# Optimization experiments

Hardware: AMD Instinct MI355X
Metric: run time of the kernel (lower is better)

## Reference

```python
import jax, jax.numpy as jnp
import numpy as np

# Model dims (GatedAttentionLayer of Qwen3.5 ANE hybrid stack)
C = 2048      # hidden_size
H = 16        # num_attention_heads
HK = 4        # num_key_value_heads
D = 128       # head_dim
ROT = 32      # rotary_dim = head_dim * partial_rotary_factor (0.25)
S = 1024      # sequence length (prefill)
CTX = 1024    # kv cache context length
N_ATTN = 6    # number of full-attention layers -> kv_cache leading dim 2*N_ATTN
EPS = 1e-6
ROPE_THETA = 1e7


def _rotate_half(x):
    h = x.shape[-1] // 2
    return jnp.concatenate([-x[..., h:], x[..., :h]], axis=-1)


def _rms_norm(x, w, eps=EPS):
    # Qwen3.5 convention: stored weight is (w - 1), applied as (1 + weight)
    r = jax.lax.rsqrt(jnp.mean(x * x, axis=-1, keepdims=True) + eps)
    return x * r * (1.0 + w)


def setup_inputs() -> dict:
    key = jax.random.key(0)
    ks = jax.random.split(key, 6)
    hidden_states = jax.random.normal(ks[0], (1, C, 1, S), jnp.float32)
    q_proj_w = jax.random.normal(ks[1], (H * 2 * D, C), jnp.float32) * 0.02  # q + gate
    k_proj_w = jax.random.normal(ks[2], (HK * D, C), jnp.float32) * 0.02
    v_proj_w = jax.random.normal(ks[3], (HK * D, C), jnp.float32) * 0.02
    o_proj_w = jax.random.normal(ks[4], (C, H * D), jnp.float32) * 0.02
    q_norm_w = jnp.zeros((D,), jnp.float32)
    k_norm_w = jnp.zeros((D,), jnp.float32)
    kv_cache = jnp.zeros((2 * N_ATTN, HK, CTX, D), jnp.float32)
    position_ids = jnp.arange(S, dtype=jnp.int32)
    # causal mask: 0 on/below diagonal, -1e9 above
    causal_mask = jnp.where(
        jnp.arange(CTX)[None, :] <= jnp.arange(S)[:, None], 0.0, -1e9
    ).astype(jnp.float32)[None, None]  # [1,1,S,CTX]
    # RoPE tables over rotary_dim
    inv_freq = 1.0 / (ROPE_THETA ** (jnp.arange(0, ROT, 2, dtype=jnp.float32) / ROT))
    t = jnp.arange(CTX, dtype=jnp.float32)
    freqs = jnp.outer(t, inv_freq)          # [CTX, ROT//2]
    emb = jnp.concatenate([freqs, freqs], -1)  # [CTX, ROT]
    cos_cached = jnp.cos(emb)
    sin_cached = jnp.sin(emb)
    return dict(hidden_states=hidden_states, q_proj_w=q_proj_w, k_proj_w=k_proj_w,
                v_proj_w=v_proj_w, o_proj_w=o_proj_w, q_norm_w=q_norm_w,
                k_norm_w=k_norm_w, kv_cache=kv_cache, causal_mask=causal_mask,
                position_ids=position_ids, cos_cached=cos_cached,
                sin_cached=sin_cached, attn_layer_idx=0)


def reference(hidden_states, q_proj_w, k_proj_w, v_proj_w, o_proj_w,
              q_norm_w, k_norm_w, kv_cache, causal_mask, position_ids,
              cos_cached, sin_cached, attn_layer_idx):
    x = hidden_states[0, :, 0, :]                     # [C, S]
    q_raw = q_proj_w @ x                              # [H*2D, S]  (1x1 Conv2d == GEMM)
    qg = q_raw.reshape(H, 2 * D, S)
    q = jnp.transpose(qg[:, :D, :], (0, 2, 1))        # [H, S, D]
    gate = jnp.transpose(qg[:, D:, :], (0, 2, 1))     # [H, S, D]
    k = jnp.transpose((k_proj_w @ x).reshape(HK, D, S), (0, 2, 1))  # [HK, S, D]
    v = jnp.transpose((v_proj_w @ x).reshape(HK, D, S), (0, 2, 1))  # [HK, S, D]

    q = _rms_norm(q, q_norm_w)
    k = _rms_norm(k, k_norm_w)

    cos = cos_cached[position_ids]   # [S, ROT]
    sin = sin_cached[position_ids]

    def rope(t):
        rot, pas = t[..., :ROT], t[..., ROT:]
        rot = rot * cos + _rotate_half(rot) * sin
        return jnp.concatenate([rot, pas], axis=-1)

    q, k = rope(q), rope(k)

    # prefill cache write at pos_start = position_ids[0]
    k_idx = 2 * attn_layer_idx
    v_idx = k_idx + 1
    pos_start = position_ids[0]
    kv_cache = jax.lax.dynamic_update_slice(kv_cache, k[None], (k_idx, 0, pos_start, 0))
    kv_cache = jax.lax.dynamic_update_slice(kv_cache, v[None], (v_idx, 0, pos_start, 0))

    g = H // HK  # GQA repeat (expand+reshape == contiguous repeat)
    k_full = jnp.repeat(kv_cache[k_idx], g, axis=0)   # [H, CTX, D]
    v_full = jnp.repeat(kv_cache[v_idx], g, axis=0)   # [H, CTX, D]

    scale = D ** -0.5
    attn = jnp.einsum('hsd,htd->hst', q, k_full) * scale + causal_mask[0]
    attn = jax.nn.softmax(attn, axis=-1)
    out = jnp.einsum('hst,htd->hsd', attn, v_full)    # [H, S, D]
    out = out * jax.nn.sigmoid(gate)
    out = jnp.transpose(out, (0, 2, 1)).reshape(H * D, S)
    output = (o_proj_w @ out)[None, :, None, :]       # [1, C, 1, S]
    return output
```

## Files before the change

### kernel.cpp

```cpp
#include <hip/hip_runtime.h>
#include <cstdint>

#define S_LEN 1024
#define C_DIM 2048
#define NH    16
#define NHK   4
#define HD    128
#define ROT   32
#define SCALE 0.08838834764831845f

typedef __bf16 bf16x8 __attribute__((ext_vector_type(8)));
typedef float floatx4 __attribute__((ext_vector_type(4)));
typedef float floatx16 __attribute__((ext_vector_type(16)));
typedef unsigned short ushortx8 __attribute__((ext_vector_type(8)));

__device__ __forceinline__ unsigned short f2bf(float f) {
  union { float f; uint32_t u; } x; x.f = f;
  uint32_t r = (x.u + 0x7fffu + ((x.u >> 16) & 1u)) >> 16;
  return (unsigned short)r;
}
__device__ __forceinline__ float bf2f(unsigned short v) {
  union { uint32_t u; float f; } x; x.u = (uint32_t)v << 16; return x.f;
}

__device__ __forceinline__ void async_copy16(const unsigned short* g, unsigned short* l) {
  __builtin_amdgcn_global_load_lds(
      (const __attribute__((address_space(1))) void*)g,
      (__attribute__((address_space(3))) void*)l,
      16, 0, 0);
}

__global__ void cast_all_kernel(const float* __restrict__ qw, const float* __restrict__ kw,
                                const float* __restrict__ vw, const float* __restrict__ ow,
                                unsigned short* __restrict__ out) {
  const int NQ = 4096 * 2048 / 4, NK = 512 * 2048 / 4, NV = 512 * 2048 / 4;
  int i = blockIdx.x * blockDim.x + threadIdx.x;
  const float* src; int j;
  if (i < NQ) { src = qw; j = i; }
  else if (i < NQ + NK) { src = kw; j = i - NQ; }
  else if (i < NQ + NK + NV) { src = vw; j = i - NQ - NK; }
  else { src = ow; j = i - NQ - NK - NV; }
  float4 v = ((const float4*)src)[j];
  ushort4 o;
  o.x = f2bf(v.x); o.y = f2bf(v.y); o.z = f2bf(v.z); o.w = f2bf(v.w);
  ((ushort4*)out)[i] = o;
}

__global__ __launch_bounds__(256)
void transpose_cast_x_kernel(const float* __restrict__ x, unsigned short* __restrict__ xT) {
  __shared__ float t[32][33];
  int st = blockIdx.x, ct = blockIdx.y;
  int c = threadIdx.x & 31, rq = threadIdx.x >> 5;
#pragma unroll
  for (int i = 0; i < 4; ++i) {
    int r = rq + i * 8;
    t[r][c] = x[(size_t)(ct * 32 + r) * S_LEN + st * 32 + c];
  }
  __syncthreads();
#pragma unroll
  for (int i = 0; i < 4; ++i) {
    int r = rq + i * 8;
    xT[(size_t)(st * 32 + r) * C_DIM + ct * 32 + c] = f2bf(t[c][r]);
  }
}

__device__ __forceinline__ void norm_rope_epi(
    floatx16 (&acc)[2], float (*pp)[32],
    const float* __restrict__ w, const int* __restrict__ pos_ids,
    const float* __restrict__ cosc, const float* __restrict__ sinc,
    unsigned short* __restrict__ outp,
    int wave, int lane, int wm, int scol0) {
  int l31 = lane & 31, half = lane >> 5;
  float s = 0.f;
#pragma unroll
  for (int mi = 0; mi < 2; ++mi)
#pragma unroll
    for (int reg = 0; reg < 16; ++reg) { float v = acc[mi][reg]; s += v * v; }
  s += __shfl_xor(s, 32);
  if (half == 0) pp[wave][l31] = s;
  __syncthreads();
  float rn = rsqrtf((pp[wave][l31] + pp[wave ^ 1][l31]) * (1.0f / 128.0f) + 1e-6f);
  int scol = scol0 + l31;
  int pos = pos_ids[scol];
#pragma unroll
  for (int mi = 0; mi < 2; ++mi) {
    bool rope = (wm == 0) && (mi == 0);
#pragma unroll
    for (int g = 0; g < 4; ++g) {
      int dbase = wm + mi * 32 + half * 4 + g * 8;
      ushort4 o;
#pragma unroll
      for (int rr = 0; rr < 4; ++rr) {
        int reg = g * 4 + rr;
        int d = dbase + rr;
        float v = acc[mi][reg] * rn * (1.0f + w[d]);
        if (rope) {
          float cv = cosc[pos * ROT + d], sv = sinc[pos * ROT + d];
          int d2 = (d < 16) ? d + 16 : d - 16;
          float pv = acc[mi][reg ^ 8] * rn * (1.0f + w[d2]);
          v = v * cv + ((d < 16) ? -pv : pv) * sv;
        }
        ((unsigned short*)&o)[rr] = f2bf(v);
      }
      *(ushort4*)&outp[(size_t)scol * HD + dbase] = o;
    }
  }
}

__global__ __launch_bounds__(256, 4)
void gemm_qkv_fused(const unsigned short* __restrict__ A,
                    const unsigned short* __restrict__ BT,
                    const float* __restrict__ qw, const float* __restrict__ kw,
                    const int* __restrict__ pos_ids,
                    const float* __restrict__ cosc, const float* __restrict__ sinc,
                    unsigned short* __restrict__ qb, unsigned short* __restrict__ kbuf,
                    unsigned short* __restrict__ vTb, unsigned short* __restrict__ sgb) {
  __shared__ unsigned short Asm[2][128 * 64];
  __shared__ unsigned short Bsm[2][64 * 64];
  __shared__ float pp[4][32];
  int tid = threadIdx.x, wave = tid >> 6, lane = tid & 63;
  int l31 = lane & 31, half = lane >> 5;
  int wm = (wave & 1) * 64, wn = (wave >> 1) * 32;
  int m0 = blockIdx.x * 128, n0 = blockIdx.y * 64;
  int r8 = lane >> 3, c8 = lane & 7;
  int arow[4], brow[2], apos[4], bpos[2];
#pragma unroll
  for (int i = 0; i < 4; ++i) { arow[i] = wave * 32 + i * 8 + r8; apos[i] = c8 ^ (arow[i] & 7); }
#pragma unroll
  for (int i = 0; i < 2; ++i) { brow[i] = wave * 16 + i * 8 + r8; bpos[i] = c8 ^ (brow[i] & 7); }
  const unsigned short* Ag = A + (size_t)m0 * C_DIM;
  const unsigned short* Bg = BT + (size_t)n0 * C_DIM;
  floatx16 acc[2];
  acc[0] = (floatx16)0.f; acc[1] = (floatx16)0.f;
  ushortx8 rA[4], rB[2];

#pragma unroll
  for (int i = 0; i < 4; ++i) rA[i] = *(const ushortx8*)(Ag + (size_t)arow[i] * C_DIM + c8 * 8);
#pragma unroll
  for (int i = 0; i < 2; ++i) rB[i] = *(const ushortx8*)(Bg + (size_t)brow[i] * C_DIM + c8 * 8);
#pragma unroll
  for (int i = 0; i < 4; ++i) *(ushortx8*)&Asm[0][arow[i] * 64 + apos[i] * 8] = rA[i];
#pragma unroll
  for (int i = 0; i < 2; ++i) *(ushortx8*)&Bsm[0][brow[i] * 64 + bpos[i] * 8] = rB[i];
  __syncthreads();

  for (int t = 0; t < 32; ++t) {
    int b = t & 1;
    if (t < 31) {
      int kt = (t + 1) * 64;
#pragma unroll
      for (int i = 0; i < 4; ++i) rA[i] = *(const ushortx8*)(Ag + (size_t)arow[i] * C_DIM + kt + c8 * 8);
#pragma unroll
      for (int i = 0; i < 2; ++i) rB[i] = *(const ushortx8*)(Bg + (size_t)brow[i] * C_DIM + kt + c8 * 8);
    }
#pragma unroll
    for (int kb = 0; kb < 4; ++kb) {
      int co = (((kb << 1) | half) ^ (l31 & 7)) << 3;
      bf16x8 a0 = *(const bf16x8*)&Asm[b][(wm + l31) * 64 + co];
      bf16x8 a1 = *(const bf16x8*)&Asm[b][(wm + 32 + l31) * 64 + co];
      bf16x8 bf = *(const bf16x8*)&Bsm[b][(wn + l31) * 64 + co];
      acc[0] = __builtin_amdgcn_mfma_f32_32x32x16_bf16(a0, bf, acc[0], 0, 0, 0);
      acc[1] = __builtin_amdgcn_mfma_f32_32x32x16_bf16(a1, bf, acc[1], 0, 0, 0);
    }
    if (t < 31) {
#pragma unroll
      for (int i = 0; i < 4; ++i) *(ushortx8*)&Asm[b ^ 1][arow[i] * 64 + apos[i] * 8] = rA[i];
#pragma unroll
      for (int i = 0; i < 2; ++i) *(ushortx8*)&Bsm[b ^ 1][brow[i] * 64 + bpos[i] * 8] = rB[i];
    }
    __syncthreads();
  }

  int scol0 = n0 + wn;
  int ty = blockIdx.x;
  if (ty < 32) {
    int h = ty >> 1;
    if ((ty & 1) == 0) {
      norm_rope_epi(acc, pp, qw, pos_ids, cosc, sinc,
                    qb + (size_t)h * S_LEN * HD, wave, lane, wm, scol0);
    } else {
      int scol = scol0 + l31;
#pragma unroll
      for (int mi = 0; mi < 2; ++mi)
#pragma unroll
        for (int g = 0; g < 4; ++g) {
          int dbase = wm + mi * 32 + half * 4 + g * 8;
          ushort4 o;
#pragma unroll
          for (int rr = 0; rr < 4; ++rr)
            ((unsigned short*)&o)[rr] = f2bf(1.0f / (1.0f + __expf(-acc[mi][g * 4 + rr])));
          *(ushort4*)&sgb[((size_t)h * S_LEN + scol) * HD + dbase] = o;
        }
    }
  } else if (ty < 36) {
    int hk = ty - 32;
    norm_rope_epi(acc, pp, kw, pos_ids, cosc, sinc,
                  kbuf + (size_t)hk * S_LEN * HD, wave, lane, wm, scol0);
  } else {
    int hk = ty - 36;
#pragma unroll
    for (int mi = 0; mi < 2; ++mi)
#pragma unroll
      for (int reg = 0; reg < 16; ++reg) {
        int d = wm + mi * 32 + (reg & 3) + 8 * (reg >> 2) + 4 * half;
        vTb[(size_t)hk * HD * S_LEN + (size_t)d * S_LEN + scol0 + l31] = f2bf(acc[mi][reg]);
      }
  }
}

__global__ __launch_bounds__(256, 4)
void gemm_oproj(const unsigned short* __restrict__ A,
                const unsigned short* __restrict__ BT,
                float* __restrict__ C) {
  __shared__ unsigned short Asm[2][128 * 64];
  __shared__ unsigned short Bsm[2][64 * 64];
  int tid = threadIdx.x, wave = tid >> 6, lane = tid & 63;
  int l31 = lane & 31, half = lane >> 5;
  int wm = (wave & 1) * 64, wn = (wave >> 1) * 32;
  int m0 = blockIdx.x * 128, n0 = blockIdx.y * 64;
  int r8 = lane >> 3, c8 = lane & 7;
  int arow[4], brow[2], apos[4], bpos[2];
#pragma unroll
  for (int i = 0; i < 4; ++i) { arow[i] = wave * 32 + i * 8 + r8; apos[i] = c8 ^ (arow[i] & 7); }
#pragma unroll
  for (int i = 0; i < 2; ++i) { brow[i] = wave * 16 + i * 8 + r8; bpos[i] = c8 ^ (brow[i] & 7); }
  const unsigned short* Ag = A + (size_t)m0 * C_DIM;
  const unsigned short* Bg = BT + (size_t)n0 * C_DIM;
  floatx16 acc[2];
  acc[0] = (floatx16)0.f; acc[1] = (floatx16)0.f;
  ushortx8 rA[4], rB[2];

#pragma unroll
  for (int i = 0; i < 4; ++i) rA[i] = *(const ushortx8*)(Ag + (size_t)arow[i] * C_DIM + c8 * 8);
#pragma unroll
  for (int i = 0; i < 2; ++i) rB[i] = *(const ushortx8*)(Bg + (size_t)brow[i] * C_DIM + c8 * 8);
#pragma unroll
  for (int i = 0; i < 4; ++i) *(ushortx8*)&Asm[0][arow[i] * 64 + apos[i] * 8] = rA[i];
#pragma unroll
  for (int i = 0; i < 2; ++i) *(ushortx8*)&Bsm[0][brow[i] * 64 + bpos[i] * 8] = rB[i];
  __syncthreads();

  for (int t = 0; t < 32; ++t) {
    int b = t & 1;
    if (t < 31) {
      int kt = (t + 1) * 64;
#pragma unroll
      for (int i = 0; i < 4; ++i) rA[i] = *(const ushortx8*)(Ag + (size_t)arow[i] * C_DIM + kt + c8 * 8);
#pragma unroll
      for (int i = 0; i < 2; ++i) rB[i] = *(const ushortx8*)(Bg + (size_t)brow[i] * C_DIM + kt + c8 * 8);
    }
#pragma unroll
    for (int kb = 0; kb < 4; ++kb) {
      int co = (((kb << 1) | half) ^ (l31 & 7)) << 3;
      bf16x8 a0 = *(const bf16x8*)&Asm[b][(wm + l31) * 64 + co];
      bf16x8 a1 = *(const bf16x8*)&Asm[b][(wm + 32 + l31) * 64 + co];
      bf16x8 bf = *(const bf16x8*)&Bsm[b][(wn + l31) * 64 + co];
      acc[0] = __builtin_amdgcn_mfma_f32_32x32x16_bf16(a0, bf, acc[0], 0, 0, 0);
      acc[1] = __builtin_amdgcn_mfma_f32_32x32x16_bf16(a1, bf, acc[1], 0, 0, 0);
    }
    if (t < 31) {
#pragma unroll
      for (int i = 0; i < 4; ++i) *(ushortx8*)&Asm[b ^ 1][arow[i] * 64 + apos[i] * 8] = rA[i];
#pragma unroll
      for (int i = 0; i < 2; ++i) *(ushortx8*)&Bsm[b ^ 1][brow[i] * 64 + bpos[i] * 8] = rB[i];
    }
    __syncthreads();
  }
#pragma unroll
  for (int mi = 0; mi < 2; ++mi)
#pragma unroll
    for (int reg = 0; reg < 16; ++reg) {
      int row = m0 + wm + mi * 32 + (reg & 3) + 8 * (reg >> 2) + 4 * half;
      C[(size_t)row * S_LEN + n0 + wn + l31] = acc[mi][reg];
    }
}

__global__ __launch_bounds__(256)
void attn_kernel(const unsigned short* __restrict__ qb,
                 const unsigned short* __restrict__ kbuf,
                 const unsigned short* __restrict__ vTb,
                 const unsigned short* __restrict__ sgb,
                 unsigned short* __restrict__ outT) {
  __shared__ __align__(16) unsigned short Ks[64 * 128];
  __shared__ __align__(16) unsigned short Vs[128 * 64];
  __shared__ __align__(16) unsigned short Ps[4][16][72];
  int h = blockIdx.x, qt = blockIdx.y;
  int s0 = qt * 64;
  int hk = h >> 2;
  int tid = threadIdx.x, wave = tid >> 6, lane = tid & 63;
  int l16 = lane & 15, quad = lane >> 4;
  int lsw = l16 & 7;

  const unsigned short* qg = qb + ((size_t)(h * S_LEN + s0 + wave * 16 + l16)) * HD;
  bf16x8 qfr[4];
#pragma unroll
  for (int kb = 0; kb < 4; ++kb)
    qfr[kb] = *(const bf16x8*)(qg + kb * 32 + quad * 8);

  float m_r[4], l_r[4];
#pragma unroll
  for (int r = 0; r < 4; ++r) { m_r[r] = -1e30f; l_r[r] = 0.f; }
  floatx4 acc_o[8];
#pragma unroll
  for (int i = 0; i < 8; ++i) acc_o[i] = (floatx4)0.f;
  int srow_base = s0 + wave * 16 + quad * 4;

  const unsigned short* kg0 = kbuf + (size_t)hk * S_LEN * HD;
  const unsigned short* vg0 = vTb + (size_t)hk * HD * S_LEN;

  int kr4 = lane >> 4, kc16 = lane & 15;
  int vr8 = lane >> 3, vc8 = lane & 7;

  for (int t = 0; t <= qt; ++t) {
    int jt = t * 64;
#pragma unroll
    for (int i = 0; i < 4; ++i) {
      int rbase = wave * 16 + i * 4;
      int row = rbase + kr4;
      int cs = kc16 ^ (row & 7);
      async_copy16(kg0 + (size_t)(jt + row) * HD + cs * 8, Ks + rbase * 128);
    }
#pragma unroll
    for (int i = 0; i < 4; ++i) {
      int rbase = wave * 32 + i * 8;
      int row = rbase + vr8;
      int cs = vc8 ^ (row & 7);
      async_copy16(vg0 + (size_t)row * S_LEN + jt + cs * 8, Vs + rbase * 64);
    }
    __syncthreads();

    floatx4 acc_s[4];
#pragma unroll
    for (int ni = 0; ni < 4; ++ni) acc_s[ni] = (floatx4)0.f;
#pragma unroll
    for (int kb = 0; kb < 4; ++kb) {
#pragma unroll
      for (int ni = 0; ni < 4; ++ni) {
        int cl = (kb * 4 + quad) ^ lsw;
        bf16x8 bk = *(const bf16x8*)&Ks[(ni * 16 + l16) * 128 + cl * 8];
        acc_s[ni] = __builtin_amdgcn_mfma_f32_16x16x32_bf16(qfr[kb], bk, acc_s[ni], 0, 0, 0);
      }
    }

    bool diag = (t == qt);
    float alpha[4];
#pragma unroll
    for (int r = 0; r < 4; ++r) {
      float scv[4];
      float mx = -1e30f;
#pragma unroll
      for (int ni = 0; ni < 4; ++ni) {
        float sv = acc_s[ni][r] * SCALE;
        if (diag) {
          int jg = jt + ni * 16 + l16;
          if (jg > srow_base + r) sv = -1e30f;
        }
        scv[ni] = sv;
        mx = fmaxf(mx, sv);
      }
#pragma unroll
      for (int off = 8; off; off >>= 1) mx = fmaxf(mx, __shfl_xor(mx, off, 16));
      float mnew = fmaxf(m_r[r], mx);
      float psv = 0.f;
#pragma unroll
      for (int ni = 0; ni < 4; ++ni) {
        float pv = (scv[ni] > -1e29f) ? __expf(scv[ni] - mnew) : 0.f;
        Ps[wave][quad * 4 + r][ni * 16 + l16] = f2bf(pv);
        psv += pv;
      }
#pragma unroll
      for (int off = 8; off; off >>= 1) psv += __shfl_xor(psv, off, 16);
      alpha[r] = __expf(m_r[r] - mnew);
      m_r[r] = mnew;
      l_r[r] = l_r[r] * alpha[r] + psv;
    }
#pragma unroll
    for (int i = 0; i < 8; ++i)
#pragma unroll
      for (int r = 0; r < 4; ++r) acc_o[i][r] *= alpha[r];
    __threadfence_block();

#pragma unroll
    for (int kb2 = 0; kb2 < 2; ++kb2) {
      bf16x8 ap = *(const bf16x8*)&Ps[wave][l16][kb2 * 32 + quad * 8];
#pragma unroll
      for (int ni2 = 0; ni2 < 8; ++ni2) {
        int cl = (kb2 * 4 + quad) ^ lsw;
        bf16x8 bv = *(const bf16x8*)&Vs[(ni2 * 16 + l16) * 64 + cl * 8];
        acc_o[ni2] = __builtin_amdgcn_mfma_f32_16x16x32_bf16(ap, bv, acc_o[ni2], 0, 0, 0);
      }
    }
    __syncthreads();
  }

#pragma unroll
  for (int r = 0; r < 4; ++r) {
    int s = srow_base + r;
    float inv = 1.0f / l_r[r];
    const unsigned short* sgp = sgb + ((size_t)h * S_LEN + s) * HD;
    unsigned short* op = outT + (size_t)s * (NH * HD) + h * HD;
#pragma unroll
    for (int ni2 = 0; ni2 < 8; ++ni2) {
      int d = ni2 * 16 + l16;
      op[d] = f2bf(acc_o[ni2][r] * inv * bf2f(sgp[d]));
    }
  }
}

extern "C" void kernel_launch(void* const* d_in, const int* in_sizes, int n_in,
                              void* d_out, int out_size, void* d_ws, size_t ws_size,
                              hipStream_t stream) {
  const float* hs       = (const float*)d_in[0];
  const float* q_proj_w = (const float*)d_in[1];
  const float* k_proj_w = (const float*)d_in[2];
  const float* v_proj_w = (const float*)d_in[3];
  const float* o_proj_w = (const float*)d_in[4];
  const float* q_norm_w = (const float*)d_in[5];
  const float* k_norm_w = (const float*)d_in[6];
  const int*   pos_ids  = (const int*)d_in[9];
  const float* cos_c    = (const float*)d_in[10];
  const float* sin_c    = (const float*)d_in[11];
  float* out = (float*)d_out;

  char* ws = (char*)d_ws;
  unsigned short* wqkv = (unsigned short*)(ws + 0);
  unsigned short* wo   = (unsigned short*)(ws + 20971520);
  unsigned short* xT   = (unsigned short*)(ws + 29360128);
  unsigned short* qb   = (unsigned short*)(ws + 33554432);
  unsigned short* kbuf = (unsigned short*)(ws + 37748736);
  unsigned short* vTb  = (unsigned short*)(ws + 38797312);
  unsigned short* sgb  = (unsigned short*)(ws + 39845888);
  unsigned short* aoT  = (unsigned short*)(ws + 44040192);

  cast_all_kernel<<<14336, 256, 0, stream>>>(q_proj_w, k_proj_w, v_proj_w, o_proj_w, wqkv);
  transpose_cast_x_kernel<<<dim3(32, 64), 256, 0, stream>>>(hs, xT);
  gemm_qkv_fused<<<dim3(40, 16), 256, 0, stream>>>(wqkv, xT, q_norm_w, k_norm_w,
                                                   pos_ids, cos_c, sin_c,
                                                   qb, kbuf, vTb, sgb);
  attn_kernel<<<dim3(16, 16), 256, 0, stream>>>(qb, kbuf, vTb, sgb, aoT);
  gemm_oproj<<<dim3(16, 16), 256, 0, stream>>>(wo, aoT, out);
}
```

Before: 246.7 us.

## Deepen GEMM global-load prefetch to two K-tiles ahead via dual register sets

Both bf16 GEMM kernels (fused QKV and output projection) now keep two register staging sets, so global loads for tile t+2 and t+3 are issued while tiles t and t+1 compute from LDS. The loop is unrolled by two with a shared MFMA macro. The aim is to hide more global-memory latency behind the MFMA work. It doubles the staging registers, which under launch_bounds(256,4) may cause spills or lower occupancy.

After: 244.4 us. No clear change (-0.9%).

```diff
diff --git a/kernel.cpp b/kernel.cpp
--- a/kernel.cpp
+++ b/kernel.cpp
@@ -106,6 +106,19 @@
     }
   }
 }
+
+#define MFMA_PHASE(BUF)                                                            \
+  {                                                                                \
+    _Pragma("unroll")                                                              \
+    for (int kb = 0; kb < 4; ++kb) {                                               \
+      int co = (((kb << 1) | half) ^ (l31 & 7)) << 3;                              \
+      bf16x8 a0 = *(const bf16x8*)&Asm[BUF][(wm + l31) * 64 + co];                 \
+      bf16x8 a1 = *(const bf16x8*)&Asm[BUF][(wm + 32 + l31) * 64 + co];            \
+      bf16x8 bf = *(const bf16x8*)&Bsm[BUF][(wn + l31) * 64 + co];                 \
+      acc[0] = __builtin_amdgcn_mfma_f32_32x32x16_bf16(a0, bf, acc[0], 0, 0, 0);   \
+      acc[1] = __builtin_amdgcn_mfma_f32_32x32x16_bf16(a1, bf, acc[1], 0, 0, 0);   \
+    }                                                                              \
+  }
 
 __global__ __launch_bounds__(256, 4)
 void gemm_qkv_fused(const unsigned short* __restrict__ A,
@@ -132,41 +145,49 @@
   const unsigned short* Bg = BT + (size_t)n0 * C_DIM;
   floatx16 acc[2];
   acc[0] = (floatx16)0.f; acc[1] = (floatx16)0.f;
-  ushortx8 rA[4], rB[2];
-
-#pragma unroll
-  for (int i = 0; i < 4; ++i) rA[i] = *(const ushortx8*)(Ag + (size_t)arow[i] * C_DIM + c8 * 8);
-#pragma unroll
-  for (int i = 0; i < 2; ++i) rB[i] = *(const ushortx8*)(Bg + (size_t)brow[i] * C_DIM + c8 * 8);
-#pragma unroll
-  for (int i = 0; i < 4; ++i) *(ushortx8*)&Asm[0][arow[i] * 64 + apos[i] * 8] = rA[i];
-#pragma unroll
-  for (int i = 0; i < 2; ++i) *(ushortx8*)&Bsm[0][brow[i] * 64 + bpos[i] * 8] = rB[i];
+  ushortx8 rA0[4], rB0[2], rA1[4], rB1[2];
+
+#pragma unroll
+  for (int i = 0; i < 4; ++i) rA0[i] = *(const ushortx8*)(Ag + (size_t)arow[i] * C_DIM + c8 * 8);
+#pragma unroll
+  for (int i = 0; i < 2; ++i) rB0[i] = *(const ushortx8*)(Bg + (size_t)brow[i] * C_DIM + c8 * 8);
+#pragma unroll
+  for (int i = 0; i < 4; ++i) rA1[i] = *(const ushortx8*)(Ag + (size_t)arow[i] * C_DIM + 64 + c8 * 8);
+#pragma unroll
+  for (int i = 0; i < 2; ++i) rB1[i] = *(const ushortx8*)(Bg + (size_t)brow[i] * C_DIM + 64 + c8 * 8);
+#pragma unroll
+  for (int i = 0; i < 4; ++i) *(ushortx8*)&Asm[0][arow[i] * 64 + apos[i] * 8] = rA0[i];
+#pragma unroll
+  for (int i = 0; i < 2; ++i) *(ushortx8*)&Bsm[0][brow[i] * 64 + bpos[i] * 8] = rB0[i];
   __syncthreads();
 
-  for (int t = 0; t < 32; ++t) {
-    int b = t & 1;
-    if (t < 31) {
-      int kt = (t + 1) * 64;
-#pragma unroll
-      for (int i = 0; i < 4; ++i) rA[i] = *(const ushortx8*)(Ag + (size_t)arow[i] * C_DIM + kt + c8 * 8);
-#pragma unroll
-      for (int i = 0; i < 2; ++i) rB[i] = *(const ushortx8*)(Bg + (size_t)brow[i] * C_DIM + kt + c8 * 8);
-    }
-#pragma unroll
-    for (int kb = 0; kb < 4; ++kb) {
-      int co = (((kb << 1) | half) ^ (l31 & 7)) << 3;
-      bf16x8 a0 = *(const bf16x8*)&Asm[b][(wm + l31) * 64 + co];
-      bf16x8 a1 = *(const bf16x8*)&Asm[b][(wm + 32 + l31) * 64 + co];
-      bf16x8 bf = *(const bf16x8*)&Bsm[b][(wn + l31) * 64 + co];
-      acc[0] = __builtin_amdgcn_mfma_f32_32x32x16_bf16(a0, bf, acc[0], 0, 0, 0);
-      acc[1] = __builtin_amdgcn_mfma_f32_32x32x16_bf16(a1, bf, acc[1], 0, 0, 0);
-    }
-    if (t < 31) {
-#pragma unroll
-      for (int i = 0; i < 4; ++i) *(ushortx8*)&Asm[b ^ 1][arow[i] * 64 + apos[i] * 8] = rA[i];
-#pragma unroll
-      for (int i = 0; i < 2; ++i) *(ushortx8*)&Bsm[b ^ 1][brow[i] * 64 + bpos[i] * 8] = rB[i];
+  for (int t = 0; t < 32; t += 2) {
+    if (t + 2 < 32) {
+      int kt = (t + 2) * 64;
+#pragma unroll
+      for (int i = 0; i < 4; ++i) rA0[i] = *(const ushortx8*)(Ag + (size_t)arow[i] * C_DIM + kt + c8 * 8);
+#pragma unroll
+      for (int i = 0; i < 2; ++i) rB0[i] = *(const ushortx8*)(Bg + (size_t)brow[i] * C_DIM + kt + c8 * 8);
+    }
+    MFMA_PHASE(0)
+#pragma unroll
+    for (int i = 0; i < 4; ++i) *(ushortx8*)&Asm[1][arow[i] * 64 + apos[i] * 8] = rA1[i];
+#pragma unroll
+    for (int i = 0; i < 2; ++i) *(ushortx8*)&Bsm[1][brow[i] * 64 + bpos[i] * 8] = rB1[i];
+    __syncthreads();
+    if (t + 3 < 32) {
+      int kt = (t + 3) * 64;
+#pragma unroll
+      for (int i = 0; i < 4; ++i) rA1[i] = *(const ushortx8*)(Ag + (size_t)arow[i] * C_DIM + kt + c8 * 8);
+#pragma unroll
+      for (int i = 0; i < 2; ++i) rB1[i] = *(const ushortx8*)(Bg + (size_t)brow[i] * C_DIM + kt + c8 * 8);
+    }
+    MFMA_PHASE(1)
+    if (t + 2 < 32) {
+#pragma unroll
+      for (int i = 0; i < 4; ++i) *(ushortx8*)&Asm[0][arow[i] * 64 + apos[i] * 8] = rA0[i];
+#pragma unroll
+      for (int i = 0; i < 2; ++i) *(ushortx8*)&Bsm[0][brow[i] * 64 + bpos[i] * 8] = rB0[i];
     }
     __syncthreads();
   }
@@ -228,41 +249,49 @@
   const unsigned short* Bg = BT + (size_t)n0 * C_DIM;
   floatx16 acc[2];
   acc[0] = (floatx16)0.f; acc[1] = (floatx16)0.f;
-  ushortx8 rA[4], rB[2];
-
-#pragma unroll
-  for (int i = 0; i < 4; ++i) rA[i] = *(const ushortx8*)(Ag + (size_t)arow[i] * C_DIM + c8 * 8);
-#pragma unroll
-  for (int i = 0; i < 2; ++i) rB[i] = *(const ushortx8*)(Bg + (size_t)brow[i] * C_DIM + c8 * 8);
-#pragma unroll
-  for (int i = 0; i < 4; ++i) *(ushortx8*)&Asm[0][arow[i] * 64 + apos[i] * 8] = rA[i];
-#pragma unroll
-  for (int i = 0; i < 2; ++i) *(ushortx8*)&Bsm[0][brow[i] * 64 + bpos[i] * 8] = rB[i];
+  ushortx8 rA0[4], rB0[2], rA1[4], rB1[2];
+
+#pragma unroll
+  for (int i = 0; i < 4; ++i) rA0[i] = *(const ushortx8*)(Ag + (size_t)arow[i] * C_DIM + c8 * 8);
+#pragma unroll
+  for (int i = 0; i < 2; ++i) rB0[i] = *(const ushortx8*)(Bg + (size_t)brow[i] * C_DIM + c8 * 8);
+#pragma unroll
+  for (int i = 0; i < 4; ++i) rA1[i] = *(const ushortx8*)(Ag + (size_t)arow[i] * C_DIM + 64 + c8 * 8);
+#pragma unroll
+  for (int i = 0; i < 2; ++i) rB1[i] = *(const ushortx8*)(Bg + (size_t)brow[i] * C_DIM + 64 + c8 * 8);
+#pragma unroll
+  for (int i = 0; i < 4; ++i) *(ushortx8*)&Asm[0][arow[i] * 64 + apos[i] * 8] = rA0[i];
+#pragma unroll
+  for (int i = 0; i < 2; ++i) *(ushortx8*)&Bsm[0][brow[i] * 64 + bpos[i] * 8] = rB0[i];
   __syncthreads();
 
-  for (int t = 0; t < 32; ++t) {
-    int b = t & 1;
-    if (t < 31) {
-      int kt = (t + 1) * 64;
-#pragma unroll
-      for (int i = 0; i < 4; ++i) rA[i] = *(const ushortx8*)(Ag + (size_t)arow[i] * C_DIM + kt + c8 * 8);
-#pragma unroll
-      for (int i = 0; i < 2; ++i) rB[i] = *(const ushortx8*)(Bg + (size_t)brow[i] * C_DIM + kt + c8 * 8);
-    }
-#pragma unroll
-    for (int kb = 0; kb < 4; ++kb) {
-      int co = (((kb << 1) | half) ^ (l31 & 7)) << 3;
-      bf16x8 a0 = *(const bf16x8*)&Asm[b][(wm + l31) * 64 + co];
-      bf16x8 a1 = *(const bf16x8*)&Asm[b][(wm + 32 + l31) * 64 + co];
-      bf16x8 bf = *(const bf16x8*)&Bsm[b][(wn + l31) * 64 + co];
-      acc[0] = __builtin_amdgcn_mfma_f32_32x32x16_bf16(a0, bf, acc[0], 0, 0, 0);
-      acc[1] = __builtin_amdgcn_mfma_f32_32x32x16_bf16(a1, bf, acc[1], 0, 0, 0);
-    }
-    if (t < 31) {
-#pragma unroll
-      for (int i = 0; i < 4; ++i) *(ushortx8*)&Asm[b ^ 1][arow[i] * 64 + apos[i] * 8] = rA[i];
-#pragma unroll
-      for (int i = 0; i < 2; ++i) *(ushortx8*)&Bsm[b ^ 1][brow[i] * 64 + bpos[i] * 8] = rB[i];
+  for (int t = 0; t < 32; t += 2) {
+    if (t + 2 < 32) {
+      int kt = (t + 2) * 64;
+#pragma unroll
+      for (int i = 0; i < 4; ++i) rA0[i] = *(const ushortx8*)(Ag + (size_t)arow[i] * C_DIM + kt + c8 * 8);
+#pragma unroll
+      for (int i = 0; i < 2; ++i) rB0[i] = *(const ushortx8*)(Bg + (size_t)brow[i] * C_DIM + kt + c8 * 8);
+    }
+    MFMA_PHASE(0)
+#pragma unroll
+    for (int i = 0; i < 4; ++i) *(ushortx8*)&Asm[1][arow[i] * 64 + apos[i] * 8] = rA1[i];
+#pragma unroll
+    for (int i = 0; i < 2; ++i) *(ushortx8*)&Bsm[1][brow[i] * 64 + bpos[i] * 8] = rB1[i];
+    __syncthreads();
+    if (t + 3 < 32) {
+      int kt = (t + 3) * 64;
+#pragma unroll
+      for (int i = 0; i < 4; ++i) rA1[i] = *(const ushortx8*)(Ag + (size_t)arow[i] * C_DIM + kt + c8 * 8);
+#pragma unroll
+      for (int i = 0; i < 2; ++i) rB1[i] = *(const ushortx8*)(Bg + (size_t)brow[i] * C_DIM + kt + c8 * 8);
+    }
+    MFMA_PHASE(1)
+    if (t + 2 < 32) {
+#pragma unroll
+      for (int i = 0; i < 4; ++i) *(ushortx8*)&Asm[0][arow[i] * 64 + apos[i] * 8] = rA0[i];
+#pragma unroll
+      for (int i = 0; i < 2; ++i) *(ushortx8*)&Bsm[0][brow[i] * 64 + bpos[i] * 8] = rB0[i];
     }
     __syncthreads();
   }
```

## Use async global-to-LDS loads and enlarge QKV GEMM tile to 128x128

Applied to the files above, without the earlier changes.

Both projection GEMMs replace register-staged global loads and explicit LDS stores with direct global_load_lds async copies, synchronised by vmcnt waits and raw barriers in a double-buffered loop. The QKV GEMM also widens its N tile from 64 to 128 so each wave computes a 2x2 set of MFMA tiles, which halves the grid and raises data reuse per loaded tile. The epilogues are extended to handle the second column tile. The cost is a larger LDS footprint and lower occupancy (launch bounds reduced to 2 and 3 blocks), and the swizzle now depends on the LDS write order of the async copy.

After: 251.3 us. No clear change (+1.9%).

```diff
diff --git a/kernel.cpp b/kernel.cpp
--- a/kernel.cpp
+++ b/kernel.cpp
@@ -29,6 +29,8 @@
       (__attribute__((address_space(3))) void*)l,
       16, 0, 0);
 }
+
+#define WAIT_VM(N) asm volatile("s_waitcnt vmcnt(" #N ")" ::: "memory")
 
 __global__ void cast_all_kernel(const float* __restrict__ qw, const float* __restrict__ kw,
                                 const float* __restrict__ vw, const float* __restrict__ ow,
@@ -64,50 +66,84 @@
   }
 }
 
-__device__ __forceinline__ void norm_rope_epi(
-    floatx16 (&acc)[2], float (*pp)[32],
+__device__ __forceinline__ void norm_rope_epi2(
+    floatx16 (&acc)[2][2], float (*pp)[64],
     const float* __restrict__ w, const int* __restrict__ pos_ids,
     const float* __restrict__ cosc, const float* __restrict__ sinc,
     unsigned short* __restrict__ outp,
     int wave, int lane, int wm, int scol0) {
   int l31 = lane & 31, half = lane >> 5;
-  float s = 0.f;
-#pragma unroll
-  for (int mi = 0; mi < 2; ++mi)
-#pragma unroll
-    for (int reg = 0; reg < 16; ++reg) { float v = acc[mi][reg]; s += v * v; }
-  s += __shfl_xor(s, 32);
-  if (half == 0) pp[wave][l31] = s;
+  float s[2] = {0.f, 0.f};
+#pragma unroll
+  for (int ni = 0; ni < 2; ++ni)
+#pragma unroll
+    for (int mi = 0; mi < 2; ++mi)
+#pragma unroll
+      for (int reg = 0; reg < 16; ++reg) { float v = acc[mi][ni][reg]; s[ni] += v * v; }
+  s[0] += __shfl_xor(s[0], 32);
+  s[1] += __shfl_xor(s[1], 32);
+  if (half == 0) { pp[wave][l31] = s[0]; pp[wave][32 + l31] = s[1]; }
   __syncthreads();
-  float rn = rsqrtf((pp[wave][l31] + pp[wave ^ 1][l31]) * (1.0f / 128.0f) + 1e-6f);
-  int scol = scol0 + l31;
-  int pos = pos_ids[scol];
-#pragma unroll
-  for (int mi = 0; mi < 2; ++mi) {
-    bool rope = (wm == 0) && (mi == 0);
-#pragma unroll
-    for (int g = 0; g < 4; ++g) {
-      int dbase = wm + mi * 32 + half * 4 + g * 8;
-      ushort4 o;
-#pragma unroll
-      for (int rr = 0; rr < 4; ++rr) {
-        int reg = g * 4 + rr;
-        int d = dbase + rr;
-        float v = acc[mi][reg] * rn * (1.0f + w[d]);
-        if (rope) {
-          float cv = cosc[pos * ROT + d], sv = sinc[pos * ROT + d];
-          int d2 = (d < 16) ? d + 16 : d - 16;
-          float pv = acc[mi][reg ^ 8] * rn * (1.0f + w[d2]);
-          v = v * cv + ((d < 16) ? -pv : pv) * sv;
+#pragma unroll
+  for (int ni = 0; ni < 2; ++ni) {
+    float rn = rsqrtf((pp[wave][ni * 32 + l31] + pp[wave ^ 1][ni * 32 + l31]) * (1.0f / 128.0f) + 1e-6f);
+    int scol = scol0 + ni * 32 + l31;
+    int pos = pos_ids[scol];
+#pragma unroll
+    for (int mi = 0; mi < 2; ++mi) {
+      bool rope = (wm == 0) && (mi == 0);
+#pragma unroll
+      for (int g = 0; g < 4; ++g) {
+        int dbase = wm + mi * 32 + half * 4 + g * 8;
+        ushort4 o;
+#pragma unroll
+        for (int rr = 0; rr < 4; ++rr) {
+          int reg = g * 4 + rr;
+          int d = dbase + rr;
+          float v = acc[mi][ni][reg] * rn * (1.0f + w[d]);
+          if (rope) {
+            float cv = cosc[pos * ROT + d], sv = sinc[pos * ROT + d];
+            int d2 = (d < 16) ? d + 16 : d - 16;
+            float pv = acc[mi][ni][reg ^ 8] * rn * (1.0f + w[d2]);
+            v = v * cv + ((d < 16) ? -pv : pv) * sv;
+          }
+          ((unsigned short*)&o)[rr] = f2bf(v);
         }
-        ((unsigned short*)&o)[rr] = f2bf(v);
-      }
-      *(ushort4*)&outp[(size_t)scol * HD + dbase] = o;
-    }
-  }
-}
-
-__global__ __launch_bounds__(256, 4)
+        *(ushort4*)&outp[(size_t)scol * HD + dbase] = o;
+      }
+    }
+  }
+}
+
+#define STAGE_QKV(BUF, KT)                                                        \
+  {                                                                               \
+    _Pragma("unroll")                                                             \
+    for (int i = 0; i < 4; ++i)                                                   \
+      async_copy16(Ag + (size_t)(wave * 32 + i * 8 + sr) * C_DIM + (KT) + scs * 8,\
+                   &Asm[BUF][(wave * 32 + i * 8) * 64]);                          \
+    _Pragma("unroll")                                                             \
+    for (int i = 0; i < 4; ++i)                                                   \
+      async_copy16(Bg + (size_t)(wave * 32 + i * 8 + sr) * C_DIM + (KT) + scs * 8,\
+                   &Bsm[BUF][(wave * 32 + i * 8) * 64]);                          \
+  }
+
+#define MFMA_QKV(BUF)                                                             \
+  {                                                                               \
+    _Pragma("unroll")                                                             \
+    for (int kb = 0; kb < 4; ++kb) {                                              \
+      int co = (((kb << 1) | half) ^ (l31 & 7)) << 3;                             \
+      bf16x8 a0 = *(const bf16x8*)&Asm[BUF][(wm + l31) * 64 + co];                \
+      bf16x8 a1 = *(const bf16x8*)&Asm[BUF][(wm + 32 + l31) * 64 + co];           \
+      bf16x8 b0 = *(const bf16x8*)&Bsm[BUF][(wn + l31) * 64 + co];                \
+      bf16x8 b1 = *(const bf16x8*)&Bsm[BUF][(wn + 32 + l31) * 64 + co];           \
+      acc[0][0] = __builtin_amdgcn_mfma_f32_32x32x16_bf16(a0, b0, acc[0][0], 0, 0, 0); \
+      acc[0][1] = __builtin_amdgcn_mfma_f32_32x32x16_bf16(a0, b1, acc[0][1], 0, 0, 0); \
+      acc[1][0] = __builtin_amdgcn_mfma_f32_32x32x16_bf16(a1, b0, acc[1][0], 0, 0, 0); \
+      acc[1][1] = __builtin_amdgcn_mfma_f32_32x32x16_bf16(a1, b1, acc[1][1], 0, 0, 0); \
+    }                                                                             \
+  }
+
+__global__ __launch_bounds__(256, 2)
 void gemm_qkv_fused(const unsigned short* __restrict__ A,
                     const unsigned short* __restrict__ BT,
                     const float* __restrict__ qw, const float* __restrict__ kw,
@@ -116,99 +152,113 @@
                     unsigned short* __restrict__ qb, unsigned short* __restrict__ kbuf,
                     unsigned short* __restrict__ vTb, unsigned short* __restrict__ sgb) {
   __shared__ unsigned short Asm[2][128 * 64];
-  __shared__ unsigned short Bsm[2][64 * 64];
-  __shared__ float pp[4][32];
+  __shared__ unsigned short Bsm[2][128 * 64];
+  __shared__ float pp[4][64];
   int tid = threadIdx.x, wave = tid >> 6, lane = tid & 63;
   int l31 = lane & 31, half = lane >> 5;
-  int wm = (wave & 1) * 64, wn = (wave >> 1) * 32;
-  int m0 = blockIdx.x * 128, n0 = blockIdx.y * 64;
-  int r8 = lane >> 3, c8 = lane & 7;
-  int arow[4], brow[2], apos[4], bpos[2];
-#pragma unroll
-  for (int i = 0; i < 4; ++i) { arow[i] = wave * 32 + i * 8 + r8; apos[i] = c8 ^ (arow[i] & 7); }
-#pragma unroll
-  for (int i = 0; i < 2; ++i) { brow[i] = wave * 16 + i * 8 + r8; bpos[i] = c8 ^ (brow[i] & 7); }
+  int wm = (wave & 1) * 64, wn = (wave >> 1) * 64;
+  int m0 = blockIdx.x * 128, n0 = blockIdx.y * 128;
+  int sr = lane >> 3, sc = lane & 7;
+  int scs = sc ^ sr;
+  (void)sc;
   const unsigned short* Ag = A + (size_t)m0 * C_DIM;
   const unsigned short* Bg = BT + (size_t)n0 * C_DIM;
-  floatx16 acc[2];
-  acc[0] = (floatx16)0.f; acc[1] = (floatx16)0.f;
-  ushortx8 rA[4], rB[2];
-
-#pragma unroll
-  for (int i = 0; i < 4; ++i) rA[i] = *(const ushortx8*)(Ag + (size_t)arow[i] * C_DIM + c8 * 8);
-#pragma unroll
-  for (int i = 0; i < 2; ++i) rB[i] = *(const ushortx8*)(Bg + (size_t)brow[i] * C_DIM + c8 * 8);
-#pragma unroll
-  for (int i = 0; i < 4; ++i) *(ushortx8*)&Asm[0][arow[i] * 64 + apos[i] * 8] = rA[i];
-#pragma unroll
-  for (int i = 0; i < 2; ++i) *(ushortx8*)&Bsm[0][brow[i] * 64 + bpos[i] * 8] = rB[i];
-  __syncthreads();
-
-  for (int t = 0; t < 32; ++t) {
-    int b = t & 1;
-    if (t < 31) {
-      int kt = (t + 1) * 64;
-#pragma unroll
-      for (int i = 0; i < 4; ++i) rA[i] = *(const ushortx8*)(Ag + (size_t)arow[i] * C_DIM + kt + c8 * 8);
-#pragma unroll
-      for (int i = 0; i < 2; ++i) rB[i] = *(const ushortx8*)(Bg + (size_t)brow[i] * C_DIM + kt + c8 * 8);
-    }
-#pragma unroll
-    for (int kb = 0; kb < 4; ++kb) {
-      int co = (((kb << 1) | half) ^ (l31 & 7)) << 3;
-      bf16x8 a0 = *(const bf16x8*)&Asm[b][(wm + l31) * 64 + co];
-      bf16x8 a1 = *(const bf16x8*)&Asm[b][(wm + 32 + l31) * 64 + co];
-      bf16x8 bf = *(const bf16x8*)&Bsm[b][(wn + l31) * 64 + co];
-      acc[0] = __builtin_amdgcn_mfma_f32_32x32x16_bf16(a0, bf, acc[0], 0, 0, 0);
-      acc[1] = __builtin_amdgcn_mfma_f32_32x32x16_bf16(a1, bf, acc[1], 0, 0, 0);
-    }
-    if (t < 31) {
-#pragma unroll
-      for (int i = 0; i < 4; ++i) *(ushortx8*)&Asm[b ^ 1][arow[i] * 64 + apos[i] * 8] = rA[i];
-#pragma unroll
-      for (int i = 0; i < 2; ++i) *(ushortx8*)&Bsm[b ^ 1][brow[i] * 64 + bpos[i] * 8] = rB[i];
-    }
-    __syncthreads();
-  }
+  floatx16 acc[2][2];
+  acc[0][0] = (floatx16)0.f; acc[0][1] = (floatx16)0.f;
+  acc[1][0] = (floatx16)0.f; acc[1][1] = (floatx16)0.f;
+
+  STAGE_QKV(0, 0)
+  STAGE_QKV(1, 64)
+
+  for (int t = 0; t < 30; t += 2) {
+    WAIT_VM(8);
+    __builtin_amdgcn_s_barrier();
+    MFMA_QKV(0)
+    __builtin_amdgcn_s_barrier();
+    STAGE_QKV(0, (t + 2) * 64)
+    WAIT_VM(8);
+    __builtin_amdgcn_s_barrier();
+    MFMA_QKV(1)
+    __builtin_amdgcn_s_barrier();
+    STAGE_QKV(1, (t + 3) * 64)
+  }
+  WAIT_VM(8);
+  __builtin_amdgcn_s_barrier();
+  MFMA_QKV(0)
+  __builtin_amdgcn_s_barrier();
+  WAIT_VM(0);
+  __builtin_amdgcn_s_barrier();
+  MFMA_QKV(1)
 
   int scol0 = n0 + wn;
   int ty = blockIdx.x;
   if (ty < 32) {
     int h = ty >> 1;
     if ((ty & 1) == 0) {
-      norm_rope_epi(acc, pp, qw, pos_ids, cosc, sinc,
-                    qb + (size_t)h * S_LEN * HD, wave, lane, wm, scol0);
+      norm_rope_epi2(acc, pp, qw, pos_ids, cosc, sinc,
+                     qb + (size_t)h * S_LEN * HD, wave, lane, wm, scol0);
     } else {
-      int scol = scol0 + l31;
-#pragma unroll
-      for (int mi = 0; mi < 2; ++mi)
-#pragma unroll
-        for (int g = 0; g < 4; ++g) {
-          int dbase = wm + mi * 32 + half * 4 + g * 8;
-          ushort4 o;
-#pragma unroll
-          for (int rr = 0; rr < 4; ++rr)
-            ((unsigned short*)&o)[rr] = f2bf(1.0f / (1.0f + __expf(-acc[mi][g * 4 + rr])));
-          *(ushort4*)&sgb[((size_t)h * S_LEN + scol) * HD + dbase] = o;
-        }
+#pragma unroll
+      for (int ni = 0; ni < 2; ++ni) {
+        int scol = scol0 + ni * 32 + l31;
+#pragma unroll
+        for (int mi = 0; mi < 2; ++mi)
+#pragma unroll
+          for (int g = 0; g < 4; ++g) {
+            int dbase = wm + mi * 32 + half * 4 + g * 8;
+            ushort4 o;
+#pragma unroll
+            for (int rr = 0; rr < 4; ++rr)
+              ((unsigned short*)&o)[rr] = f2bf(1.0f / (1.0f + __expf(-acc[mi][ni][g * 4 + rr])));
+            *(ushort4*)&sgb[((size_t)h * S_LEN + scol) * HD + dbase] = o;
+          }
+      }
     }
   } else if (ty < 36) {
     int hk = ty - 32;
-    norm_rope_epi(acc, pp, kw, pos_ids, cosc, sinc,
-                  kbuf + (size_t)hk * S_LEN * HD, wave, lane, wm, scol0);
+    norm_rope_epi2(acc, pp, kw, pos_ids, cosc, sinc,
+                   kbuf + (size_t)hk * S_LEN * HD, wave, lane, wm, scol0);
   } else {
     int hk = ty - 36;
 #pragma unroll
-    for (int mi = 0; mi < 2; ++mi)
-#pragma unroll
-      for (int reg = 0; reg < 16; ++reg) {
-        int d = wm + mi * 32 + (reg & 3) + 8 * (reg >> 2) + 4 * half;
-        vTb[(size_t)hk * HD * S_LEN + (size_t)d * S_LEN + scol0 + l31] = f2bf(acc[mi][reg]);
-      }
-  }
-}
-
-__global__ __launch_bounds__(256, 4)
+    for (int ni = 0; ni < 2; ++ni)
+#pragma unroll
+      for (int mi = 0; mi < 2; ++mi)
+#pragma unroll
+        for (int reg = 0; reg < 16; ++reg) {
+          int d = wm + mi * 32 + (reg & 3) + 8 * (reg >> 2) + 4 * half;
+          vTb[(size_t)hk * HD * S_LEN + (size_t)d * S_LEN + scol0 + ni * 32 + l31] =
+              f2bf(acc[mi][ni][reg]);
+        }
+  }
+}
+
+#define STAGE_O(BUF, KT)                                                          \
+  {                                                                               \
+    _Pragma("unroll")                                                             \
+    for (int i = 0; i < 4; ++i)                                                   \
+      async_copy16(Ag + (size_t)(wave * 32 + i * 8 + sr) * C_DIM + (KT) + scs * 8,\
+                   &Asm[BUF][(wave * 32 + i * 8) * 64]);                          \
+    _Pragma("unroll")                                                             \
+    for (int i = 0; i < 2; ++i)                                                   \
+      async_copy16(Bg + (size_t)(wave * 16 + i * 8 + sr) * C_DIM + (KT) + scs * 8,\
+                   &Bsm[BUF][(wave * 16 + i * 8) * 64]);                          \
+  }
+
+#define MFMA_O(BUF)                                                               \
+  {                                                                               \
+    _Pragma("unroll")                                                             \
+    for (int kb = 0; kb < 4; ++kb) {                                              \
+      int co = (((kb << 1) | half) ^ (l31 & 7)) << 3;                             \
+      bf16x8 a0 = *(const bf16x8*)&Asm[BUF][(wm + l31) * 64 + co];                \
+      bf16x8 a1 = *(const bf16x8*)&Asm[BUF][(wm + 32 + l31) * 64 + co];           \
+      bf16x8 bf = *(const bf16x8*)&Bsm[BUF][(wn + l31) * 64 + co];                \
+      acc[0] = __builtin_amdgcn_mfma_f32_32x32x16_bf16(a0, bf, acc[0], 0, 0, 0);  \
+      acc[1] = __builtin_amdgcn_mfma_f32_32x32x16_bf16(a1, bf, acc[1], 0, 0, 0);  \
+    }                                                                             \
+  }
+
+__global__ __launch_bounds__(256, 3)
 void gemm_oproj(const unsigned short* __restrict__ A,
                 const unsigned short* __restrict__ BT,
                 float* __restrict__ C) {
@@ -218,54 +268,36 @@
   int l31 = lane & 31, half = lane >> 5;
   int wm = (wave & 1) * 64, wn = (wave >> 1) * 32;
   int m0 = blockIdx.x * 128, n0 = blockIdx.y * 64;
-  int r8 = lane >> 3, c8 = lane & 7;
-  int arow[4], brow[2], apos[4], bpos[2];
-#pragma unroll
-  for (int i = 0; i < 4; ++i) { arow[i] = wave * 32 + i * 8 + r8; apos[i] = c8 ^ (arow[i] & 7); }
-#pragma unroll
-  for (int i = 0; i < 2; ++i) { brow[i] = wave * 16 + i * 8 + r8; bpos[i] = c8 ^ (brow[i] & 7); }
+  int sr = lane >> 3;
+  int scs = (lane & 7) ^ sr;
   const unsigned short* Ag = A + (size_t)m0 * C_DIM;
   const unsigned short* Bg = BT + (size_t)n0 * C_DIM;
   floatx16 acc[2];
   acc[0] = (floatx16)0.f; acc[1] = (floatx16)0.f;
-  ushortx8 rA[4], rB[2];
-
-#pragma unroll
-  for (int i = 0; i < 4; ++i) rA[i] = *(const ushortx8*)(Ag + (size_t)arow[i] * C_DIM + c8 * 8);
-#pragma unroll
-  for (int i = 0; i < 2; ++i) rB[i] = *(const ushortx8*)(Bg + (size_t)brow[i] * C_DIM + c8 * 8);
-#pragma unroll
-  for (int i = 0; i < 4; ++i) *(ushortx8*)&Asm[0][arow[i] * 64 + apos[i] * 8] = rA[i];
-#pragma unroll
-  for (int i = 0; i < 2; ++i) *(ushortx8*)&Bsm[0][brow[i] * 64 + bpos[i] * 8] = rB[i];
-  __syncthreads();
-
-  for (int t = 0; t < 32; ++t) {
-    int b = t & 1;
-    if (t < 31) {
-      int kt = (t + 1) * 64;
-#pragma unroll
-      for (int i = 0; i < 4; ++i) rA[i] = *(const ushortx8*)(Ag + (size_t)arow[i] * C_DIM + kt + c8 * 8);
-#pragma unroll
-      for (int i = 0; i < 2; ++i) rB[i] = *(const ushortx8*)(Bg + (size_t)brow[i] * C_DIM + kt + c8 * 8);
-    }
-#pragma unroll
-    for (int kb = 0; kb < 4; ++kb) {
-      int co = (((kb << 1) | half) ^ (l31 & 7)) << 3;
-      bf16x8 a0 = *(const bf16x8*)&Asm[b][(wm + l31) * 64 + co];
-      bf16x8 a1 = *(const bf16x8*)&Asm[b][(wm + 32 + l31) * 64 + co];
-      bf16x8 bf = *(const bf16x8*)&Bsm[b][(wn + l31) * 64 + co];
-      acc[0] = __builtin_amdgcn_mfma_f32_32x32x16_bf16(a0, bf, acc[0], 0, 0, 0);
-      acc[1] = __builtin_amdgcn_mfma_f32_32x32x16_bf16(a1, bf, acc[1], 0, 0, 0);
-    }
-    if (t < 31) {
-#pragma unroll
-      for (int i = 0; i < 4; ++i) *(ushortx8*)&Asm[b ^ 1][arow[i] * 64 + apos[i] * 8] = rA[i];
-#pragma unroll
-      for (int i = 0; i < 2; ++i) *(ushortx8*)&Bsm[b ^ 1][brow[i] * 64 + bpos[i] * 8] = rB[i];
-    }
-    __syncthreads();
-  }
+
+  STAGE_O(0, 0)
+  STAGE_O(1, 64)
+
+  for (int t = 0; t < 30; t += 2) {
+    WAIT_VM(6);
+    __builtin_amdgcn_s_barrier();
+    MFMA_O(0)
+    __builtin_amdgcn_s_barrier();
+    STAGE_O(0, (t + 2) * 64)
+    WAIT_VM(6);
+    __builtin_amdgcn_s_barrier();
+    MFMA_O(1)
+    __builtin_amdgcn_s_barrier();
+    STAGE_O(1, (t + 3) * 64)
+  }
+  WAIT_VM(6);
+  __builtin_amdgcn_s_barrier();
+  MFMA_O(0)
+  __builtin_amdgcn_s_barrier();
+  WAIT_VM(0);
+  __builtin_amdgcn_s_barrier();
+  MFMA_O(1)
+
 #pragma unroll
   for (int mi = 0; mi < 2; ++mi)
 #pragma unroll
@@ -434,9 +466,9 @@
 
   cast_all_kernel<<<14336, 256, 0, stream>>>(q_proj_w, k_proj_w, v_proj_w, o_proj_w, wqkv);
   transpose_cast_x_kernel<<<dim3(32, 64), 256, 0, stream>>>(hs, xT);
-  gemm_qkv_fused<<<dim3(40, 16), 256, 0, stream>>>(wqkv, xT, q_norm_w, k_norm_w,
-                                                   pos_ids, cos_c, sin_c,
-                                                   qb, kbuf, vTb, sgb);
+  gemm_qkv_fused<<<dim3(40, 8), 256, 0, stream>>>(wqkv, xT, q_norm_w, k_norm_w,
+                                                  pos_ids, cos_c, sin_c,
+                                                  qb, kbuf, vTb, sgb);
   attn_kernel<<<dim3(16, 16), 256, 0, stream>>>(qb, kbuf, vTb, sgb, aoT);
   gemm_oproj<<<dim3(16, 16), 256, 0, stream>>>(wo, aoT, out);
 }
```
